# Performance work log

Measured on AMD Instinct MI355X. Metric: run time of the kernel, lower is better.

Reference implementation:

```python
import jax, jax.numpy as jnp
import numpy as np

V0, V1 = 0.1, 0.2  # SSD encode/decode variances
LEVEL_WS = [160, 80, 40, 20, 10, 5]
BOUNDS = [0, 25600, 32000, 33600, 34000, 34100, 34125]
A_TOTAL = 34125
CLS_W, LOC_W = 1.0, 2.0

def _to_cxcywh(a):
    return np.stack([(a[:, 0] + a[:, 2]) / 2.0, (a[:, 1] + a[:, 3]) / 2.0,
                     a[:, 2] - a[:, 0], a[:, 3] - a[:, 1]], 1)

def _decode(d, anc):
    xy = anc[:, :2] + d[:, :2] * V0 * anc[:, 2:]
    wh = anc[:, 2:] * np.exp(d[:, 2:] * V1)
    return np.concatenate([xy - wh / 2.0, xy + wh / 2.0], 1)

def _encode(anc, gt):
    gcx = (gt[:, 0] + gt[:, 2]) / 2.0; gcy = (gt[:, 1] + gt[:, 3]) / 2.0
    gw = gt[:, 2] - gt[:, 0]; gh = gt[:, 3] - gt[:, 1]
    return np.stack([(gcx - anc[:, 0]) / (anc[:, 2] * V0),
                     (gcy - anc[:, 1]) / (anc[:, 3] * V0),
                     np.log(np.maximum(gw, 1e-6) / anc[:, 2]) / V1,
                     np.log(np.maximum(gh, 1e-6) / anc[:, 3]) / V1], 1)

def _relabel(conf, bbox_targets, anchors):
    # Faithful mirror of the torch.no_grad() relabel loop: per-image per-level
    # decode, unique-with-counts, center-distance top-k, sigmoid-score sort,
    # scatter relabel. Data-dependent shapes, so done in numpy (no grads flow here).
    conf = np.asarray(conf); bt = np.array(bbox_targets, copy=True); anc = np.asarray(anchors)
    tanc = _to_cxcywh(anc)
    labels = bt[:, :, -1].copy()
    for b in range(conf.shape[0]):
        pos = bt[b, :, -1] == 1
        uniq = []
        for li in range(6):
            s, e = BOUNDS[li], BOUNDS[li + 1]
            m = pos[s:e]
            dec = _decode(bt[b, s:e][m][:, :4], tanc[s:e][m])
            uniq.append(np.unique(np.round(dec, 3), axis=0, return_counts=True))
        start_idx, end_idx, tmp_w = -25600, 0, 160.0
        for li, (u, c) in enumerate(uniq):
            if li > 4:
                continue
            if u.shape[0] == 0:
                continue
            max_num = int(c.max())
            start_idx += int(tmp_w ** 2); end_idx += int(tmp_w ** 2); tmp_w /= 2.0
            s, e = start_idx, end_idx
            ctr = tanc[s:e, :2]
            for ti in range(u.shape[0]):
                n_match = int(c[ti])
                if n_match == max_num:
                    continue
                gt = u[ti]
                dist = np.hypot(ctr[:, 0] - (gt[0] + gt[2]) / 2.0, ctr[:, 1] - (gt[1] + gt[3]) / 2.0)
                cand = np.argsort(dist, kind='stable')[:max_num]
                scores = 1.0 / (1.0 + np.exp(-conf[b, s + cand, 0]))
                order = np.argsort(scores, kind='stable')
                rel = cand[order[-(max_num - n_match):]] + s
                rel = rel[labels[b, rel] != 1]
                if rel.shape[0] == 0:
                    continue
                bt[b, rel, :4] = _encode(tanc[rel], np.repeat(gt[None, :], rel.shape[0], 0))
                bt[b, rel, 4] = 1.0
                labels[b, rel] = 1.0
    return labels.astype(np.float32), bt.astype(np.float32)

def _losses(conf, loc, labels, bt):
    # cls: sigmoid BCE-with-logits summed, normalized by num positives
    # loc: smooth-L1 on encoded deltas over positive anchors, same normalization
    tgt = (labels == 1).astype(conf.dtype)
    z = conf[..., 0]
    bce = jnp.maximum(z, 0) - z * tgt + jnp.log1p(jnp.exp(-jnp.abs(z)))
    num_pos = jnp.maximum(tgt.sum(), 1.0)
    cls_loss = CLS_W * bce.sum() / num_pos
    d = loc - bt[..., :4]
    sl1 = jnp.where(jnp.abs(d) < 1.0, 0.5 * d * d, jnp.abs(d) - 0.5)
    loc_loss = LOC_W * (sl1 * tgt[..., None]).sum() / num_pos
    return cls_loss, loc_loss, cls_loss + loc_loss

def setup_inputs() -> dict:
    rng = np.random.RandomState(0)
    B, NGT = 16, 8
    anchors = []
    for w in LEVEL_WS:
        stride = 640.0 / w
        t = (np.arange(w) + 0.5) * stride
        cy, cx = np.meshgrid(t, t, indexing='ij')
        cx = cx.reshape(-1); cy = cy.reshape(-1); sz = 4.0 * stride
        anchors.append(np.stack([cx - sz / 2, cy - sz / 2, cx + sz / 2, cy + sz / 2], 1))
    anchors = np.concatenate(anchors, 0).astype(np.float32)  # [34125, 4]
    tanc = _to_cxcywh(anchors)
    bt = np.zeros((B, A_TOTAL, 5), np.float32)
    bt[:, :, :4] = rng.randn(B, A_TOTAL, 4).astype(np.float32) * 0.1
    gts = np.zeros((B, NGT, 4), np.float32)
    for b in range(B):
        for g in range(NGT):
            cx, cy = rng.uniform(64, 576, 2); sz = rng.uniform(16, 256)
            gt = np.array([cx - sz / 2, cy - sz / 2, cx + sz / 2, cy + sz / 2], np.float32)
            gts[b, g] = gt
            li = int(rng.randint(0, 5))
            s, e = BOUNDS[li], BOUNDS[li + 1]
            k = int(rng.randint(2, 20))
            idx = rng.choice(e - s, size=k, replace=False) + s
            bt[b, idx, :4] = _encode(tanc[idx], np.repeat(gt[None, :], k, 0)).astype(np.float32)
            bt[b, idx, 4] = 1.0
    conf = rng.randn(B, A_TOTAL, 1).astype(np.float32)
    loc = (rng.randn(B, A_TOTAL, 4) * 0.1).astype(np.float32)
    return {"conf": jnp.asarray(conf), "loc": jnp.asarray(loc),
            "bbox_targets": jnp.asarray(bt), "anchors": jnp.asarray(anchors),
            "bbox_labels_list": jnp.asarray(gts)}

def reference(conf, loc, bbox_targets, anchors, bbox_labels_list):
    labels, bt = _relabel(conf, bbox_targets, anchors)
    return _losses(conf, loc, jnp.asarray(labels), jnp.asarray(bt))
```

## Files before the change

kernel.cpp:

```cpp
#include <hip/hip_runtime.h>
#include <cstdint>
#include <cstddef>

#define A_TOTAL 34125
#define BATCH 16
#define NBA (BATCH * A_TOTAL)
#define SBT 1024
#define PT2 25
#define NB 1024
#define CAND 768
#define NSEG (BATCH * 5)
#define CCAP 16384
#define SELGRID 160
#define SCAN_GRID 1024
#define SCAN_THR 256

__device__ __constant__ int d_bounds[7] = {0, 25600, 32000, 33600, 34000, 34100, 34125};

#define MAXU 48
#define MAXPOS 512
#define MAXC 32
#define CLAIM_NONE 0x7FFFFFFF

__global__ __launch_bounds__(SCAN_THR)
void scan_kernel(const float* __restrict__ bt,
                 const float* __restrict__ anchors,
                 const float* __restrict__ conf,
                 const float* __restrict__ loc,
                 int* __restrict__ claim,
                 uint8_t* __restrict__ posmap,
                 float* __restrict__ part,
                 int* __restrict__ ccnt,
                 int* __restrict__ done_cnt,
                 float2* __restrict__ ctr) {
    const int tid = threadIdx.x;
    const int gtid = blockIdx.x * blockDim.x + tid;
    const int gsz = gridDim.x * blockDim.x;
    if (gtid == 0) { *ccnt = 0; *done_cnt = 0; }

    int4* c4 = (int4*)claim;
    for (int i = gtid; i < NBA / 4; i += gsz)
        c4[i] = make_int4(CLAIM_NONE, CLAIM_NONE, CLAIM_NONE, CLAIM_NONE);
    for (int a = gtid; a < A_TOTAL; a += gsz) {
        const float4 ar = reinterpret_cast<const float4*>(anchors)[a];
        ctr[a] = make_float2((ar.x + ar.z) / 2.0f, (ar.y + ar.w) / 2.0f);
    }

    float bce = 0.0f, pos = 0.0f, l1 = 0.0f;

    const float4* cf4 = (const float4*)conf;
    for (int i = gtid; i < NBA / 4; i += gsz) {
        const float4 z4 = cf4[i];
        const float zz[4] = {z4.x, z4.y, z4.z, z4.w};
        #pragma unroll
        for (int c = 0; c < 4; ++c) {
            const float z = zz[c];
            bce += fmaxf(z, 0.0f) + log1pf(expf(-fabsf(z)));
        }
    }

    const float4* btv = (const float4*)bt;
    const int nchunk = NBA * 5 / 4;
    for (int f4 = gtid; f4 < nchunk; f4 += gsz) {
        const float4 v = btv[f4];
        const unsigned g0 = (unsigned)f4 * 4u;
        const unsigned m = g0 % 5u;
        if (m != 0u) {
            const unsigned c = 4u - m;
            const float val = (c == 0u) ? v.x : (c == 1u) ? v.y : (c == 2u) ? v.z : v.w;
            const unsigned i = (g0 + c) / 5u;
            const bool p = (val == 1.0f);
            posmap[i] = p ? 1 : 0;
            if (p) {
                bce -= conf[i];
                pos += 1.0f;
                const float* tp = bt + (size_t)i * 5u;
                const float4 lv4 = reinterpret_cast<const float4*>(loc)[i];
                const float dv[4] = {lv4.x - tp[0], lv4.y - tp[1],
                                     lv4.z - tp[2], lv4.w - tp[3]};
                #pragma unroll
                for (int cc = 0; cc < 4; ++cc) {
                    const float ad = fabsf(dv[cc]);
                    l1 += (ad < 1.0f) ? 0.5f * dv[cc] * dv[cc] : ad - 0.5f;
                }
            }
        }
    }

    for (int off = 32; off > 0; off >>= 1) {
        bce += __shfl_down(bce, off);
        pos += __shfl_down(pos, off);
        l1  += __shfl_down(l1, off);
    }
    __shared__ float sb[3][4];
    const int wid = tid >> 6, lane = tid & 63;
    if (lane == 0) { sb[0][wid] = bce; sb[1][wid] = pos; sb[2][wid] = l1; }
    __syncthreads();
    if (tid == 0) {
        float B = 0, P = 0, L = 0;
        #pragma unroll
        for (int w = 0; w < 4; ++w) { B += sb[0][w]; P += sb[1][w]; L += sb[2][w]; }
        part[blockIdx.x * 3 + 0] = B;
        part[blockIdx.x * 3 + 1] = P;
        part[blockIdx.x * 3 + 2] = L;
    }
}

__global__ __launch_bounds__(256)
void dedup_kernel(const float* __restrict__ bt,
                  const float* __restrict__ anchors,
                  const uint8_t* __restrict__ posmap,
                  float* __restrict__ uq,
                  int* __restrict__ uc,
                  int* __restrict__ nu_out,
                  int* __restrict__ mn_out,
                  int* __restrict__ wl,
                  int* __restrict__ wlc)
{
    const int b = blockIdx.x / 5;
    const int lv = blockIdx.x % 5;
    const int seg = blockIdx.x;
    const unsigned bA = (unsigned)b * A_TOTAL;
    const int tid = threadIdx.x;

    __shared__ int s_pos[MAXPOS];
    __shared__ float t0[MAXPOS], t1[MAXPOS], t2[MAXPOS], t3[MAXPOS];
    __shared__ int s_cnt[MAXPOS];
    __shared__ uint8_t s_rep[MAXPOS];
    __shared__ int s_ucs[MAXU];
    __shared__ int s_np, s_nu;

    if (tid == 0) { s_np = 0; s_nu = 0; }
    __syncthreads();

    {
        const unsigned gs = bA + (unsigned)d_bounds[lv];
        const unsigned ge = bA + (unsigned)d_bounds[lv + 1];
        const unsigned astart = (gs + 15u) & ~15u;
        const unsigned aend_raw = ge & ~15u;
        const unsigned hend = min(astart, ge);
        for (unsigned g = gs + tid; g < hend; g += blockDim.x)
            if (posmap[g]) {
                int p = atomicAdd(&s_np, 1);
                if (p < MAXPOS) s_pos[p] = (int)(g - bA);
            }
        if (aend_raw > astart) {
            const uint4* pm4 = (const uint4*)(posmap + astart);
            const unsigned n16 = (aend_raw - astart) >> 4;
            for (unsigned c = tid; c < n16; c += blockDim.x) {
                const uint4 v = pm4[c];
                if (v.x | v.y | v.z | v.w) {
                    const unsigned base = astart + (c << 4);
                    const unsigned wv[4] = {v.x, v.y, v.z, v.w};
                    #pragma unroll
                    for (int w = 0; w < 4; ++w) {
                        #pragma unroll
                        for (int byi = 0; byi < 4; ++byi) {
                            if ((wv[w] >> (8 * byi)) & 0xffu) {
                                int p = atomicAdd(&s_np, 1);
                                if (p < MAXPOS)
                                    s_pos[p] = (int)(base + 4u * w + byi - bA);
                            }
                        }
                    }
                }
            }
            for (unsigned g = aend_raw + tid; g < ge; g += blockDim.x)
                if (posmap[g]) {
                    int p = atomicAdd(&s_np, 1);
                    if (p < MAXPOS) s_pos[p] = (int)(g - bA);
                }
        }
    }
    __syncthreads();
    const int np_ = min(s_np, MAXPOS);

    for (int p = tid; p < np_; p += blockDim.x) {
        int a = s_pos[p];
        const float* ar = anchors + (size_t)a * 4;
        float acx = (ar[0] + ar[2]) / 2.0f;
        float acy = (ar[1] + ar[3]) / 2.0f;
        float aw = ar[2] - ar[0];
        float ah = ar[3] - ar[1];
        const float* dd = bt + ((size_t)bA + a) * 5;
        float cx = acx + (dd[0] * 0.1f) * aw;
        float cy = acy + (dd[1] * 0.1f) * ah;
        float w = aw * expf(dd[2] * 0.2f);
        float h = ah * expf(dd[3] * 0.2f);
        t0[p] = rintf((cx - w / 2.0f) * 1000.0f) / 1000.0f;
        t1[p] = rintf((cy - h / 2.0f) * 1000.0f) / 1000.0f;
        t2[p] = rintf((cx + w / 2.0f) * 1000.0f) / 1000.0f;
        t3[p] = rintf((cy + h / 2.0f) * 1000.0f) / 1000.0f;
    }
    __syncthreads();

    for (int p = tid; p < np_; p += blockDim.x) {
        const float p0 = t0[p], p1 = t1[p], p2 = t2[p], p3 = t3[p];
        int cnt = 0, firstq = np_;
        for (int q = 0; q < np_; ++q) {
            bool eq = (t0[q] == p0) && (t1[q] == p1) && (t2[q] == p2) && (t3[q] == p3);
            if (eq) { cnt++; if (q < firstq) firstq = q; }
        }
        s_cnt[p] = cnt;
        bool rep = (firstq == p);
        s_rep[p] = rep ? 1 : 0;
        if (rep) atomicAdd(&s_nu, 1);
    }
    __syncthreads();

    float* uqp = uq + (size_t)seg * MAXU * 4;
    int* ucp = uc + (size_t)seg * MAXU;
    for (int p = tid; p < np_; p += blockDim.x) {
        if (!s_rep[p]) continue;
        const float p0 = t0[p], p1 = t1[p], p2 = t2[p], p3 = t3[p];
        int rank = 0;
        for (int q = 0; q < np_; ++q) {
            if (!s_rep[q]) continue;
            float q0 = t0[q], q1 = t1[q], q2 = t2[q], q3 = t3[q];
            bool lt = (q0 < p0) || (q0 == p0 && (q1 < p1 ||
                      (q1 == p1 && (q2 < p2 || (q2 == p2 && q3 < p3)))));
            if (lt) rank++;
        }
        if (rank < MAXU) {
            uqp[rank * 4 + 0] = p0; uqp[rank * 4 + 1] = p1;
            uqp[rank * 4 + 2] = p2; uqp[rank * 4 + 3] = p3;
            ucp[rank] = s_cnt[p];
            s_ucs[rank] = s_cnt[p];
        }
    }
    __syncthreads();

    if (tid == 0) {
        const int nu = min(s_nu, MAXU);
        nu_out[seg] = nu;
        int mn = 0;
        for (int j = 0; j < nu; ++j) mn = max(mn, s_ucs[j]);
        mn_out[seg] = mn;
        int n = 0;
        for (int ti = 0; ti < nu; ++ti)
            if (s_ucs[ti] != mn) wl[seg * MAXU + n++] = seg * MAXU + ti;
        wlc[seg] = n;
    }
}

__global__ __launch_bounds__(SBT)
void select_kernel(const float* __restrict__ conf,
                   const float* __restrict__ loc,
                   const float* __restrict__ bt,
                   const float* __restrict__ anchors,
                   const float2* __restrict__ ctr,
                   const float* __restrict__ uq,
                   const int* __restrict__ uc,
                   const int* __restrict__ nu_,
                   const int* __restrict__ mn_,
                   const int* __restrict__ wl,
                   const int* __restrict__ wlc,
                   int* __restrict__ claim,
                   unsigned* __restrict__ clist,
                   int* __restrict__ ccnt,
                   int* __restrict__ done_cnt,
                   const float* __restrict__ part,
                   float* __restrict__ out) {
    const int tid = threadIdx.x;

    __shared__ int s_hist[NB];
    __shared__ unsigned long long s_cand[CAND];
    __shared__ unsigned long long s_srt[MAXC];
    __shared__ float s_sc[MAXC];
    __shared__ int s_c, s_B, s_last;

    for (int w = blockIdx.x; ; w += gridDim.x) {
        int cum = 0, ent = -1;
        for (int i = 0; i < NSEG; ++i) {
            int c = wlc[i];
            if (ent < 0 && w < cum + c) ent = wl[i * MAXU + (w - cum)];
            cum += c;
        }
        if (w >= cum) break;

        const int ti = ent % MAXU;
        const int sg = ent / MAXU;
        const int li = sg % 5;
        const int b  = sg / 5;

        int nus[5];
        #pragma unroll
        for (int l = 0; l < 5; ++l) nus[l] = nu_[b * 5 + l];

        int s = -25600;
        float tmpw = 160.0f;
        for (int l = 0; l <= li; ++l) {
            if (nus[l] != 0) { s += (int)(tmpw * tmpw); tmpw *= 0.5f; }
        }

        const int mn = mn_[sg];
        const int cnt = uc[(size_t)sg * MAXU + ti];
        const int need = mn - cnt;
        const int K = min(mn, MAXC);
        const unsigned bA = (unsigned)b * A_TOTAL;

        const float* g = uq + ((size_t)sg * MAXU + ti) * 4;
        const float gcx = (g[0] + g[2]) / 2.0f;
        const float gcy = (g[1] + g[3]) / 2.0f;

        float cxr[PT2], cyr[PT2];
        #pragma unroll
        for (int i = 0; i < PT2; ++i) {
            const float2 c = ctr[s + tid + (i << 10)];
            cxr[i] = c.x;
            cyr[i] = c.y;
        }

        s_hist[tid] = 0;
        if (tid == 0) s_c = 0;
        __syncthreads();

        #pragma unroll
        for (int i = 0; i < PT2; ++i) {
            float d = hypotf(cxr[i] - gcx, cyr[i] - gcy);
            int bin = min(NB - 1, (int)d);
            atomicAdd(&s_hist[bin], 1);
        }
        __syncthreads();

        if (tid < 64) {
            const int base = tid << 4;
            int prt[16], psum = 0;
            #pragma unroll
            for (int i = 0; i < 16; ++i) { prt[i] = s_hist[base + i]; psum += prt[i]; }
            int run = psum;
            #pragma unroll
            for (int off = 1; off < 64; off <<= 1) {
                int o = __shfl_up(run, off);
                if (tid >= off) run += o;
            }
            const int excl = run - psum;
            if (excl < K && excl + psum >= K) {
                int c = excl, bs = base + 15;
                for (int i = 0; i < 16; ++i) { c += prt[i]; if (c >= K) { bs = base + i; break; } }
                s_B = bs;
            }
        }
        __syncthreads();
        const int B = s_B;

        #pragma unroll
        for (int i = 0; i < PT2; ++i) {
            float d = hypotf(cxr[i] - gcx, cyr[i] - gcy);
            int bin = min(NB - 1, (int)d);
            if (bin <= B) {
                int p = atomicAdd(&s_c, 1);
                if (p < CAND)
                    s_cand[p] = (((unsigned long long)__float_as_uint(d)) << 32) |
                                (unsigned)(tid + (i << 10));
            }
        }
        __syncthreads();
        const int C = min(s_c, CAND);

        if (tid < C) {
            const unsigned long long mykey = s_cand[tid];
            int rank = 0;
            for (int j = 0; j < C; ++j) rank += (s_cand[j] < mykey) ? 1 : 0;
            if (rank < K) s_srt[rank] = mykey;
        }
        __syncthreads();

        if (tid < K) {
            const int o = (int)(s_srt[tid] & 0xffffffffULL);
            const float z = conf[bA + s + o];
            s_sc[tid] = 1.0f / (1.0f + expf(-z));
        }
        __syncthreads();

        if (tid < K) {
            const float my = s_sc[tid];
            int r = 0;
            for (int j = 0; j < K; ++j) {
                const float oj = s_sc[j];
                r += (oj > my || (oj == my && j > tid)) ? 1 : 0;
            }
            if (r < need) {
                const int o = (int)(s_srt[tid] & 0xffffffffULL);
                const int idx = (int)(bA + s + o);
                const int seq = li * MAXU + ti;
                atomicMin(&claim[idx], seq);
                int p = atomicAdd(ccnt, 1);
                if (p < CCAP)
                    atomicExch(&clist[p], ((unsigned)idx << 8) | (unsigned)seq);
            }
        }
        __syncthreads();
    }

    __syncthreads();
    if (tid == 0) {
        __threadfence();
        s_last = (atomicAdd(done_cnt, 1) == gridDim.x - 1) ? 1 : 0;
    }
    __syncthreads();
    if (!s_last) return;

    float bce = 0.0f, pos = 0.0f, l1 = 0.0f;
    const int cn = min(atomicAdd(ccnt, 0), CCAP);
    for (int e = tid; e < cn; e += blockDim.x) {
        const unsigned pack = atomicAdd(&clist[e], 0u);
        const int idx = (int)(pack >> 8);
        const int seq = (int)(pack & 0xffu);
        if (atomicAdd(&claim[idx], 0) != seq) continue;
        if (bt[(size_t)idx * 5 + 4] == 1.0f) continue;
        bce -= conf[idx];
        pos += 1.0f;
        const int uli = seq / MAXU;
        const int uti = seq - uli * MAXU;
        const int b = idx / A_TOTAL;
        const int a = idx - b * A_TOTAL;
        const float* g = uq + ((size_t)(b * 5 + uli) * MAXU + uti) * 4;
        const float g0 = g[0], g1 = g[1], g2 = g[2], g3 = g[3];
        const float gcx = (g0 + g2) / 2.0f, gcy = (g1 + g3) / 2.0f;
        const float gw = g2 - g0, gh = g3 - g1;
        const float* ar = anchors + (size_t)a * 4;
        const float acx = (ar[0] + ar[2]) / 2.0f;
        const float acy = (ar[1] + ar[3]) / 2.0f;
        const float aw = ar[2] - ar[0];
        const float ah = ar[3] - ar[1];
        float ep[4];
        ep[0] = (gcx - acx) / (aw * 0.1f);
        ep[1] = (gcy - acy) / (ah * 0.1f);
        ep[2] = logf(fmaxf(gw, 1e-6f) / aw) / 0.2f;
        ep[3] = logf(fmaxf(gh, 1e-6f) / ah) / 0.2f;
        const float4 lvv = reinterpret_cast<const float4*>(loc)[idx];
        const float lvf[4] = {lvv.x, lvv.y, lvv.z, lvv.w};
        #pragma unroll
        for (int c = 0; c < 4; ++c) {
            const float dd = lvf[c] - ep[c];
            const float ad = fabsf(dd);
            l1 += (ad < 1.0f) ? 0.5f * dd * dd : ad - 0.5f;
        }
    }

    if (tid < SCAN_GRID) {
        bce += part[tid * 3 + 0];
        pos += part[tid * 3 + 1];
        l1  += part[tid * 3 + 2];
    }

    for (int off = 32; off > 0; off >>= 1) {
        bce += __shfl_down(bce, off);
        pos += __shfl_down(pos, off);
        l1  += __shfl_down(l1, off);
    }
    __shared__ float sb[3][16];
    const int wid = tid >> 6, lane = tid & 63;
    if (lane == 0) { sb[0][wid] = bce; sb[1][wid] = pos; sb[2][wid] = l1; }
    __syncthreads();
    if (tid == 0) {
        float B = 0, P = 0, L = 0;
        #pragma unroll
        for (int w = 0; w < 16; ++w) { B += sb[0][w]; P += sb[1][w]; L += sb[2][w]; }
        const double a0 = (double)B;
        const double a1 = (double)P;
        const double a2 = (double)L;
        const double np_ = a1 > 1.0 ? a1 : 1.0;
        const double cls = a0 / np_;
        const double lcl = 2.0 * a2 / np_;
        out[0] = (float)cls;
        out[1] = (float)lcl;
        out[2] = (float)(cls + lcl);
    }
}

extern "C" void kernel_launch(void* const* d_in, const int* in_sizes, int n_in,
                              void* d_out, int out_size, void* d_ws, size_t ws_size,
                              hipStream_t stream) {
    const float* conf    = (const float*)d_in[0];
    const float* loc     = (const float*)d_in[1];
    const float* bt      = (const float*)d_in[2];
    const float* anchors = (const float*)d_in[3];
    float* out = (float*)d_out;

    char* ws = (char*)d_ws;
    size_t off = 0;
    int* ccnt       = (int*)(ws + off);
    int* done_cnt   = (int*)(ws + 32);     off += 64;
    float* part     = (float*)(ws + off);  off += (size_t)SCAN_GRID * 3 * sizeof(float);
    int* claim      = (int*)(ws + off);    off += (size_t)NBA * sizeof(int);
    uint8_t* posmap = (uint8_t*)(ws + off); off += ((size_t)NBA + 63) & ~63ull;
    float* uq       = (float*)(ws + off);  off += (size_t)NSEG * MAXU * 4 * sizeof(float);
    int* uc         = (int*)(ws + off);    off += (size_t)NSEG * MAXU * sizeof(int);
    int* nu_        = (int*)(ws + off);    off += (size_t)NSEG * sizeof(int);
    int* mn_        = (int*)(ws + off);    off += (size_t)NSEG * sizeof(int);
    int* wl         = (int*)(ws + off);    off += (size_t)NSEG * MAXU * sizeof(int);
    int* wlc        = (int*)(ws + off);    off += ((size_t)NSEG * sizeof(int) + 15) & ~15ull;
    unsigned* clist = (unsigned*)(ws + off); off += (size_t)CCAP * sizeof(unsigned);
    float2* ctr     = (float2*)(ws + off); off += (size_t)A_TOTAL * sizeof(float2);

    scan_kernel<<<SCAN_GRID, SCAN_THR, 0, stream>>>(bt, anchors, conf, loc, claim,
                                                    posmap, part, ccnt, done_cnt, ctr);
    dedup_kernel<<<NSEG, 256, 0, stream>>>(bt, anchors, posmap, uq, uc, nu_, mn_,
                                           wl, wlc);
    select_kernel<<<SELGRID, SBT, 0, stream>>>(conf, loc, bt, anchors, ctr, uq, uc,
                                               nu_, mn_, wl, wlc, claim, clist, ccnt,
                                               done_cnt, part, out);
}
```

Before: 57.15 us.

## Fuse scan, dedup and select kernels into one cooperative kernel with grid syncs

Merges the three separate kernel launches into a single cooperative mega-kernel of 128 blocks by 1024 threads. Grid-wide barriers replace the kernel boundaries, and the last-block done-counter finalisation becomes block 0 running after a final grid sync. This is meant to remove launch overhead and inter-kernel gaps. In exchange, the streaming scan phase now runs on fewer threads, dedup still occupies only 80 blocks, and the select phase runs on 128 blocks instead of 160.

```diff
diff --git a/kernel.cpp b/kernel.cpp
--- a/kernel.cpp
+++ b/kernel.cpp
@@ -1,19 +1,20 @@
 #include <hip/hip_runtime.h>
+#include <hip/hip_cooperative_groups.h>
 #include <cstdint>
 #include <cstddef>
+
+namespace cg = cooperative_groups;
 
 #define A_TOTAL 34125
 #define BATCH 16
 #define NBA (BATCH * A_TOTAL)
-#define SBT 1024
+#define THR 1024
+#define GRID 128
 #define PT2 25
 #define NB 1024
 #define CAND 768
 #define NSEG (BATCH * 5)
 #define CCAP 16384
-#define SELGRID 160
-#define SCAN_GRID 1024
-#define SCAN_THR 256
 
 __device__ __constant__ int d_bounds[7] = {0, 25600, 32000, 33600, 34000, 34100, 34125};
 
@@ -22,8 +23,8 @@
 #define MAXC 32
 #define CLAIM_NONE 0x7FFFFFFF
 
-__global__ __launch_bounds__(SCAN_THR)
-void scan_kernel(const float* __restrict__ bt,
+__global__ __launch_bounds__(THR)
+void mega_kernel(const float* __restrict__ bt,
                  const float* __restrict__ anchors,
                  const float* __restrict__ conf,
                  const float* __restrict__ loc,
@@ -31,97 +32,20 @@
                  uint8_t* __restrict__ posmap,
                  float* __restrict__ part,
                  int* __restrict__ ccnt,
-                 int* __restrict__ done_cnt,
-                 float2* __restrict__ ctr) {
+                 float2* __restrict__ ctr,
+                 float* __restrict__ uq,
+                 int* __restrict__ uc,
+                 int* __restrict__ nu_,
+                 int* __restrict__ mn_,
+                 int* __restrict__ wl,
+                 int* __restrict__ wlc,
+                 unsigned* __restrict__ clist,
+                 float* __restrict__ out)
+{
+    cg::grid_group grid = cg::this_grid();
     const int tid = threadIdx.x;
     const int gtid = blockIdx.x * blockDim.x + tid;
     const int gsz = gridDim.x * blockDim.x;
-    if (gtid == 0) { *ccnt = 0; *done_cnt = 0; }
-
-    int4* c4 = (int4*)claim;
-    for (int i = gtid; i < NBA / 4; i += gsz)
-        c4[i] = make_int4(CLAIM_NONE, CLAIM_NONE, CLAIM_NONE, CLAIM_NONE);
-    for (int a = gtid; a < A_TOTAL; a += gsz) {
-        const float4 ar = reinterpret_cast<const float4*>(anchors)[a];
-        ctr[a] = make_float2((ar.x + ar.z) / 2.0f, (ar.y + ar.w) / 2.0f);
-    }
-
-    float bce = 0.0f, pos = 0.0f, l1 = 0.0f;
-
-    const float4* cf4 = (const float4*)conf;
-    for (int i = gtid; i < NBA / 4; i += gsz) {
-        const float4 z4 = cf4[i];
-        const float zz[4] = {z4.x, z4.y, z4.z, z4.w};
-        #pragma unroll
-        for (int c = 0; c < 4; ++c) {
-            const float z = zz[c];
-            bce += fmaxf(z, 0.0f) + log1pf(expf(-fabsf(z)));
-        }
-    }
-
-    const float4* btv = (const float4*)bt;
-    const int nchunk = NBA * 5 / 4;
-    for (int f4 = gtid; f4 < nchunk; f4 += gsz) {
-        const float4 v = btv[f4];
-        const unsigned g0 = (unsigned)f4 * 4u;
-        const unsigned m = g0 % 5u;
-        if (m != 0u) {
-            const unsigned c = 4u - m;
-            const float val = (c == 0u) ? v.x : (c == 1u) ? v.y : (c == 2u) ? v.z : v.w;
-            const unsigned i = (g0 + c) / 5u;
-            const bool p = (val == 1.0f);
-            posmap[i] = p ? 1 : 0;
-            if (p) {
-                bce -= conf[i];
-                pos += 1.0f;
-                const float* tp = bt + (size_t)i * 5u;
-                const float4 lv4 = reinterpret_cast<const float4*>(loc)[i];
-                const float dv[4] = {lv4.x - tp[0], lv4.y - tp[1],
-                                     lv4.z - tp[2], lv4.w - tp[3]};
-                #pragma unroll
-                for (int cc = 0; cc < 4; ++cc) {
-                    const float ad = fabsf(dv[cc]);
-                    l1 += (ad < 1.0f) ? 0.5f * dv[cc] * dv[cc] : ad - 0.5f;
-                }
-            }
-        }
-    }
-
-    for (int off = 32; off > 0; off >>= 1) {
-        bce += __shfl_down(bce, off);
-        pos += __shfl_down(pos, off);
-        l1  += __shfl_down(l1, off);
-    }
-    __shared__ float sb[3][4];
-    const int wid = tid >> 6, lane = tid & 63;
-    if (lane == 0) { sb[0][wid] = bce; sb[1][wid] = pos; sb[2][wid] = l1; }
-    __syncthreads();
-    if (tid == 0) {
-        float B = 0, P = 0, L = 0;
-        #pragma unroll
-        for (int w = 0; w < 4; ++w) { B += sb[0][w]; P += sb[1][w]; L += sb[2][w]; }
-        part[blockIdx.x * 3 + 0] = B;
-        part[blockIdx.x * 3 + 1] = P;
-        part[blockIdx.x * 3 + 2] = L;
-    }
-}
-
-__global__ __launch_bounds__(256)
-void dedup_kernel(const float* __restrict__ bt,
-                  const float* __restrict__ anchors,
-                  const uint8_t* __restrict__ posmap,
-                  float* __restrict__ uq,
-                  int* __restrict__ uc,
-                  int* __restrict__ nu_out,
-                  int* __restrict__ mn_out,
-                  int* __restrict__ wl,
-                  int* __restrict__ wlc)
-{
-    const int b = blockIdx.x / 5;
-    const int lv = blockIdx.x % 5;
-    const int seg = blockIdx.x;
-    const unsigned bA = (unsigned)b * A_TOTAL;
-    const int tid = threadIdx.x;
 
     __shared__ int s_pos[MAXPOS];
     __shared__ float t0[MAXPOS], t1[MAXPOS], t2[MAXPOS], t3[MAXPOS];
@@ -129,145 +53,205 @@
     __shared__ uint8_t s_rep[MAXPOS];
     __shared__ int s_ucs[MAXU];
     __shared__ int s_np, s_nu;
-
-    if (tid == 0) { s_np = 0; s_nu = 0; }
-    __syncthreads();
+    __shared__ int s_hist[NB];
+    __shared__ unsigned long long s_cand[CAND];
+    __shared__ unsigned long long s_srt[MAXC];
+    __shared__ float s_sc[MAXC];
+    __shared__ int s_c, s_B;
+    __shared__ float sb[3][16];
+
+    if (gtid == 0) *ccnt = 0;
 
     {
-        const unsigned gs = bA + (unsigned)d_bounds[lv];
-        const unsigned ge = bA + (unsigned)d_bounds[lv + 1];
-        const unsigned astart = (gs + 15u) & ~15u;
-        const unsigned aend_raw = ge & ~15u;
-        const unsigned hend = min(astart, ge);
-        for (unsigned g = gs + tid; g < hend; g += blockDim.x)
-            if (posmap[g]) {
-                int p = atomicAdd(&s_np, 1);
-                if (p < MAXPOS) s_pos[p] = (int)(g - bA);
-            }
-        if (aend_raw > astart) {
-            const uint4* pm4 = (const uint4*)(posmap + astart);
-            const unsigned n16 = (aend_raw - astart) >> 4;
-            for (unsigned c = tid; c < n16; c += blockDim.x) {
-                const uint4 v = pm4[c];
-                if (v.x | v.y | v.z | v.w) {
-                    const unsigned base = astart + (c << 4);
-                    const unsigned wv[4] = {v.x, v.y, v.z, v.w};
+        int4* c4 = (int4*)claim;
+        for (int i = gtid; i < NBA / 4; i += gsz)
+            c4[i] = make_int4(CLAIM_NONE, CLAIM_NONE, CLAIM_NONE, CLAIM_NONE);
+        for (int a = gtid; a < A_TOTAL; a += gsz) {
+            const float4 ar = reinterpret_cast<const float4*>(anchors)[a];
+            ctr[a] = make_float2((ar.x + ar.z) / 2.0f, (ar.y + ar.w) / 2.0f);
+        }
+
+        float bce = 0.0f, pos = 0.0f, l1 = 0.0f;
+
+        const float4* cf4 = (const float4*)conf;
+        for (int i = gtid; i < NBA / 4; i += gsz) {
+            const float4 z4 = cf4[i];
+            const float zz[4] = {z4.x, z4.y, z4.z, z4.w};
+            #pragma unroll
+            for (int c = 0; c < 4; ++c) {
+                const float z = zz[c];
+                bce += fmaxf(z, 0.0f) + log1pf(expf(-fabsf(z)));
+            }
+        }
+
+        const float4* btv = (const float4*)bt;
+        const int nchunk = NBA * 5 / 4;
+        for (int f4 = gtid; f4 < nchunk; f4 += gsz) {
+            const float4 v = btv[f4];
+            const unsigned g0 = (unsigned)f4 * 4u;
+            const unsigned m = g0 % 5u;
+            if (m != 0u) {
+                const unsigned c = 4u - m;
+                const float val = (c == 0u) ? v.x : (c == 1u) ? v.y : (c == 2u) ? v.z : v.w;
+                const unsigned i = (g0 + c) / 5u;
+                const bool p = (val == 1.0f);
+                posmap[i] = p ? 1 : 0;
+                if (p) {
+                    bce -= conf[i];
+                    pos += 1.0f;
+                    const float* tp = bt + (size_t)i * 5u;
+                    const float4 lv4 = reinterpret_cast<const float4*>(loc)[i];
+                    const float dv[4] = {lv4.x - tp[0], lv4.y - tp[1],
+                                         lv4.z - tp[2], lv4.w - tp[3]};
                     #pragma unroll
-                    for (int w = 0; w < 4; ++w) {
+                    for (int cc = 0; cc < 4; ++cc) {
+                        const float ad = fabsf(dv[cc]);
+                        l1 += (ad < 1.0f) ? 0.5f * dv[cc] * dv[cc] : ad - 0.5f;
+                    }
+                }
+            }
+        }
+
+        for (int off = 32; off > 0; off >>= 1) {
+            bce += __shfl_down(bce, off);
+            pos += __shfl_down(pos, off);
+            l1  += __shfl_down(l1, off);
+        }
+        const int wid = tid >> 6, lane = tid & 63;
+        if (lane == 0) { sb[0][wid] = bce; sb[1][wid] = pos; sb[2][wid] = l1; }
+        __syncthreads();
+        if (tid == 0) {
+            float B = 0, P = 0, L = 0;
+            #pragma unroll
+            for (int w = 0; w < 16; ++w) { B += sb[0][w]; P += sb[1][w]; L += sb[2][w]; }
+            part[blockIdx.x * 3 + 0] = B;
+            part[blockIdx.x * 3 + 1] = P;
+            part[blockIdx.x * 3 + 2] = L;
+        }
+    }
+
+    grid.sync();
+
+    if (blockIdx.x < NSEG) {
+        const int b = blockIdx.x / 5;
+        const int lv = blockIdx.x % 5;
+        const int seg = blockIdx.x;
+        const unsigned bA = (unsigned)b * A_TOTAL;
+
+        if (tid == 0) { s_np = 0; s_nu = 0; }
+        __syncthreads();
+
+        {
+            const unsigned gs = bA + (unsigned)d_bounds[lv];
+            const unsigned ge = bA + (unsigned)d_bounds[lv + 1];
+            const unsigned astart = (gs + 15u) & ~15u;
+            const unsigned aend_raw = ge & ~15u;
+            const unsigned hend = min(astart, ge);
+            for (unsigned g = gs + tid; g < hend; g += blockDim.x)
+                if (posmap[g]) {
+                    int p = atomicAdd(&s_np, 1);
+                    if (p < MAXPOS) s_pos[p] = (int)(g - bA);
+                }
+            if (aend_raw > astart) {
+                const uint4* pm4 = (const uint4*)(posmap + astart);
+                const unsigned n16 = (aend_raw - astart) >> 4;
+                for (unsigned c = tid; c < n16; c += blockDim.x) {
+                    const uint4 v = pm4[c];
+                    if (v.x | v.y | v.z | v.w) {
+                        const unsigned base = astart + (c << 4);
+                        const unsigned wv[4] = {v.x, v.y, v.z, v.w};
                         #pragma unroll
-                        for (int byi = 0; byi < 4; ++byi) {
-                            if ((wv[w] >> (8 * byi)) & 0xffu) {
-                                int p = atomicAdd(&s_np, 1);
-                                if (p < MAXPOS)
-                                    s_pos[p] = (int)(base + 4u * w + byi - bA);
+                        for (int w = 0; w < 4; ++w) {
+                            #pragma unroll
+                            for (int byi = 0; byi < 4; ++byi) {
+                                if ((wv[w] >> (8 * byi)) & 0xffu) {
+                                    int p = atomicAdd(&s_np, 1);
+                                    if (p < MAXPOS)
+                                        s_pos[p] = (int)(base + 4u * w + byi - bA);
+                                }
                             }
                         }
                     }
                 }
-            }
-            for (unsigned g = aend_raw + tid; g < ge; g += blockDim.x)
-                if (posmap[g]) {
-                    int p = atomicAdd(&s_np, 1);
-                    if (p < MAXPOS) s_pos[p] = (int)(g - bA);
-                }
+                for (unsigned g = aend_raw + tid; g < ge; g += blockDim.x)
+                    if (posmap[g]) {
+                        int p = atomicAdd(&s_np, 1);
+                        if (p < MAXPOS) s_pos[p] = (int)(g - bA);
+                    }
+            }
+        }
+        __syncthreads();
+        const int np_ = min(s_np, MAXPOS);
+
+        for (int p = tid; p < np_; p += blockDim.x) {
+            int a = s_pos[p];
+            const float* ar = anchors + (size_t)a * 4;
+            float acx = (ar[0] + ar[2]) / 2.0f;
+            float acy = (ar[1] + ar[3]) / 2.0f;
+            float aw = ar[2] - ar[0];
+            float ah = ar[3] - ar[1];
+            const float* dd = bt + ((size_t)bA + a) * 5;
+            float cx = acx + (dd[0] * 0.1f) * aw;
+            float cy = acy + (dd[1] * 0.1f) * ah;
+            float w = aw * expf(dd[2] * 0.2f);
+            float h = ah * expf(dd[3] * 0.2f);
+            t0[p] = rintf((cx - w / 2.0f) * 1000.0f) / 1000.0f;
+            t1[p] = rintf((cy - h / 2.0f) * 1000.0f) / 1000.0f;
+            t2[p] = rintf((cx + w / 2.0f) * 1000.0f) / 1000.0f;
+            t3[p] = rintf((cy + h / 2.0f) * 1000.0f) / 1000.0f;
+        }
+        __syncthreads();
+
+        for (int p = tid; p < np_; p += blockDim.x) {
+            const float p0 = t0[p], p1 = t1[p], p2 = t2[p], p3 = t3[p];
+            int cnt = 0, firstq = np_;
+            for (int q = 0; q < np_; ++q) {
+                bool eq = (t0[q] == p0) && (t1[q] == p1) && (t2[q] == p2) && (t3[q] == p3);
+                if (eq) { cnt++; if (q < firstq) firstq = q; }
+            }
+            s_cnt[p] = cnt;
+            bool rep = (firstq == p);
+            s_rep[p] = rep ? 1 : 0;
+            if (rep) atomicAdd(&s_nu, 1);
+        }
+        __syncthreads();
+
+        float* uqp = uq + (size_t)seg * MAXU * 4;
+        int* ucp = uc + (size_t)seg * MAXU;
+        for (int p = tid; p < np_; p += blockDim.x) {
+            if (!s_rep[p]) continue;
+            const float p0 = t0[p], p1 = t1[p], p2 = t2[p], p3 = t3[p];
+            int rank = 0;
+            for (int q = 0; q < np_; ++q) {
+                if (!s_rep[q]) continue;
+                float q0 = t0[q], q1 = t1[q], q2 = t2[q], q3 = t3[q];
+                bool lt = (q0 < p0) || (q0 == p0 && (q1 < p1 ||
+                          (q1 == p1 && (q2 < p2 || (q2 == p2 && q3 < p3)))));
+                if (lt) rank++;
+            }
+            if (rank < MAXU) {
+                uqp[rank * 4 + 0] = p0; uqp[rank * 4 + 1] = p1;
+                uqp[rank * 4 + 2] = p2; uqp[rank * 4 + 3] = p3;
+                ucp[rank] = s_cnt[p];
+                s_ucs[rank] = s_cnt[p];
+            }
+        }
+        __syncthreads();
+
+        if (tid == 0) {
+            const int nu = min(s_nu, MAXU);
+            nu_[seg] = nu;
+            int mn = 0;
+            for (int j = 0; j < nu; ++j) mn = max(mn, s_ucs[j]);
+            mn_[seg] = mn;
+            int n = 0;
+            for (int ti = 0; ti < nu; ++ti)
+                if (s_ucs[ti] != mn) wl[seg * MAXU + n++] = seg * MAXU + ti;
+            wlc[seg] = n;
         }
     }
-    __syncthreads();
-    const int np_ = min(s_np, MAXPOS);
-
-    for (int p = tid; p < np_; p += blockDim.x) {
-        int a = s_pos[p];
-        const float* ar = anchors + (size_t)a * 4;
-        float acx = (ar[0] + ar[2]) / 2.0f;
-        float acy = (ar[1] + ar[3]) / 2.0f;
-        float aw = ar[2] - ar[0];
-        float ah = ar[3] - ar[1];
-        const float* dd = bt + ((size_t)bA + a) * 5;
-        float cx = acx + (dd[0] * 0.1f) * aw;
-        float cy = acy + (dd[1] * 0.1f) * ah;
-        float w = aw * expf(dd[2] * 0.2f);
-        float h = ah * expf(dd[3] * 0.2f);
-        t0[p] = rintf((cx - w / 2.0f) * 1000.0f) / 1000.0f;
-        t1[p] = rintf((cy - h / 2.0f) * 1000.0f) / 1000.0f;
-        t2[p] = rintf((cx + w / 2.0f) * 1000.0f) / 1000.0f;
-        t3[p] = rintf((cy + h / 2.0f) * 1000.0f) / 1000.0f;
-    }
-    __syncthreads();
-
-    for (int p = tid; p < np_; p += blockDim.x) {
-        const float p0 = t0[p], p1 = t1[p], p2 = t2[p], p3 = t3[p];
-        int cnt = 0, firstq = np_;
-        for (int q = 0; q < np_; ++q) {
-            bool eq = (t0[q] == p0) && (t1[q] == p1) && (t2[q] == p2) && (t3[q] == p3);
-            if (eq) { cnt++; if (q < firstq) firstq = q; }
-        }
-        s_cnt[p] = cnt;
-        bool rep = (firstq == p);
-        s_rep[p] = rep ? 1 : 0;
-        if (rep) atomicAdd(&s_nu, 1);
-    }
-    __syncthreads();
-
-    float* uqp = uq + (size_t)seg * MAXU * 4;
-    int* ucp = uc + (size_t)seg * MAXU;
-    for (int p = tid; p < np_; p += blockDim.x) {
-        if (!s_rep[p]) continue;
-        const float p0 = t0[p], p1 = t1[p], p2 = t2[p], p3 = t3[p];
-        int rank = 0;
-        for (int q = 0; q < np_; ++q) {
-            if (!s_rep[q]) continue;
-            float q0 = t0[q], q1 = t1[q], q2 = t2[q], q3 = t3[q];
-            bool lt = (q0 < p0) || (q0 == p0 && (q1 < p1 ||
-                      (q1 == p1 && (q2 < p2 || (q2 == p2 && q3 < p3)))));
-            if (lt) rank++;
-        }
-        if (rank < MAXU) {
-            uqp[rank * 4 + 0] = p0; uqp[rank * 4 + 1] = p1;
-            uqp[rank * 4 + 2] = p2; uqp[rank * 4 + 3] = p3;
-            ucp[rank] = s_cnt[p];
-            s_ucs[rank] = s_cnt[p];
-        }
-    }
-    __syncthreads();
-
-    if (tid == 0) {
-        const int nu = min(s_nu, MAXU);
-        nu_out[seg] = nu;
-        int mn = 0;
-        for (int j = 0; j < nu; ++j) mn = max(mn, s_ucs[j]);
-        mn_out[seg] = mn;
-        int n = 0;
-        for (int ti = 0; ti < nu; ++ti)
-            if (s_ucs[ti] != mn) wl[seg * MAXU + n++] = seg * MAXU + ti;
-        wlc[seg] = n;
-    }
-}
-
-__global__ __launch_bounds__(SBT)
-void select_kernel(const float* __restrict__ conf,
-                   const float* __restrict__ loc,
-                   const float* __restrict__ bt,
-                   const float* __restrict__ anchors,
-                   const float2* __restrict__ ctr,
-                   const float* __restrict__ uq,
-                   const int* __restrict__ uc,
-                   const int* __restrict__ nu_,
-                   const int* __restrict__ mn_,
-                   const int* __restrict__ wl,
-                   const int* __restrict__ wlc,
-                   int* __restrict__ claim,
-                   unsigned* __restrict__ clist,
-                   int* __restrict__ ccnt,
-                   int* __restrict__ done_cnt,
-                   const float* __restrict__ part,
-                   float* __restrict__ out) {
-    const int tid = threadIdx.x;
-
-    __shared__ int s_hist[NB];
-    __shared__ unsigned long long s_cand[CAND];
-    __shared__ unsigned long long s_srt[MAXC];
-    __shared__ float s_sc[MAXC];
-    __shared__ int s_c, s_B, s_last;
+
+    grid.sync();
 
     for (int w = blockIdx.x; ; w += gridDim.x) {
         int cum = 0, ent = -1;
@@ -393,80 +377,77 @@
         __syncthreads();
     }
 
-    __syncthreads();
-    if (tid == 0) {
-        __threadfence();
-        s_last = (atomicAdd(done_cnt, 1) == gridDim.x - 1) ? 1 : 0;
-    }
-    __syncthreads();
-    if (!s_last) return;
-
-    float bce = 0.0f, pos = 0.0f, l1 = 0.0f;
-    const int cn = min(atomicAdd(ccnt, 0), CCAP);
-    for (int e = tid; e < cn; e += blockDim.x) {
-        const unsigned pack = atomicAdd(&clist[e], 0u);
-        const int idx = (int)(pack >> 8);
-        const int seq = (int)(pack & 0xffu);
-        if (atomicAdd(&claim[idx], 0) != seq) continue;
-        if (bt[(size_t)idx * 5 + 4] == 1.0f) continue;
-        bce -= conf[idx];
-        pos += 1.0f;
-        const int uli = seq / MAXU;
-        const int uti = seq - uli * MAXU;
-        const int b = idx / A_TOTAL;
-        const int a = idx - b * A_TOTAL;
-        const float* g = uq + ((size_t)(b * 5 + uli) * MAXU + uti) * 4;
-        const float g0 = g[0], g1 = g[1], g2 = g[2], g3 = g[3];
-        const float gcx = (g0 + g2) / 2.0f, gcy = (g1 + g3) / 2.0f;
-        const float gw = g2 - g0, gh = g3 - g1;
-        const float* ar = anchors + (size_t)a * 4;
-        const float acx = (ar[0] + ar[2]) / 2.0f;
-        const float acy = (ar[1] + ar[3]) / 2.0f;
-        const float aw = ar[2] - ar[0];
-        const float ah = ar[3] - ar[1];
-        float ep[4];
-        ep[0] = (gcx - acx) / (aw * 0.1f);
-        ep[1] = (gcy - acy) / (ah * 0.1f);
-        ep[2] = logf(fmaxf(gw, 1e-6f) / aw) / 0.2f;
-        ep[3] = logf(fmaxf(gh, 1e-6f) / ah) / 0.2f;
-        const float4 lvv = reinterpret_cast<const float4*>(loc)[idx];
-        const float lvf[4] = {lvv.x, lvv.y, lvv.z, lvv.w};
-        #pragma unroll
-        for (int c = 0; c < 4; ++c) {
-            const float dd = lvf[c] - ep[c];
-            const float ad = fabsf(dd);
-            l1 += (ad < 1.0f) ? 0.5f * dd * dd : ad - 0.5f;
-        }
-    }
-
-    if (tid < SCAN_GRID) {
-        bce += part[tid * 3 + 0];
-        pos += part[tid * 3 + 1];
-        l1  += part[tid * 3 + 2];
-    }
-
-    for (int off = 32; off > 0; off >>= 1) {
-        bce += __shfl_down(bce, off);
-        pos += __shfl_down(pos, off);
-        l1  += __shfl_down(l1, off);
-    }
-    __shared__ float sb[3][16];
-    const int wid = tid >> 6, lane = tid & 63;
-    if (lane == 0) { sb[0][wid] = bce; sb[1][wid] = pos; sb[2][wid] = l1; }
-    __syncthreads();
-    if (tid == 0) {
-        float B = 0, P = 0, L = 0;
-        #pragma unroll
-        for (int w = 0; w < 16; ++w) { B += sb[0][w]; P += sb[1][w]; L += sb[2][w]; }
-        const double a0 = (double)B;
-        const double a1 = (double)P;
-        const double a2 = (double)L;
-        const double np_ = a1 > 1.0 ? a1 : 1.0;
-        const double cls = a0 / np_;
-        const double lcl = 2.0 * a2 / np_;
-        out[0] = (float)cls;
-        out[1] = (float)lcl;
-        out[2] = (float)(cls + lcl);
+    grid.sync();
+
+    if (blockIdx.x != 0) return;
+
+    {
+        float bce = 0.0f, pos = 0.0f, l1 = 0.0f;
+        const int cn = min(atomicAdd(ccnt, 0), CCAP);
+        for (int e = tid; e < cn; e += blockDim.x) {
+            const unsigned pack = atomicAdd(&clist[e], 0u);
+            const int idx = (int)(pack >> 8);
+            const int seq = (int)(pack & 0xffu);
+            if (atomicAdd(&claim[idx], 0) != seq) continue;
+            if (bt[(size_t)idx * 5 + 4] == 1.0f) continue;
+            bce -= conf[idx];
+            pos += 1.0f;
+            const int uli = seq / MAXU;
+            const int uti = seq - uli * MAXU;
+            const int b = idx / A_TOTAL;
+            const int a = idx - b * A_TOTAL;
+            const float* g = uq + ((size_t)(b * 5 + uli) * MAXU + uti) * 4;
+            const float g0 = g[0], g1 = g[1], g2 = g[2], g3 = g[3];
+            const float gcx = (g0 + g2) / 2.0f, gcy = (g1 + g3) / 2.0f;
+            const float gw = g2 - g0, gh = g3 - g1;
+            const float* ar = anchors + (size_t)a * 4;
+            const float acx = (ar[0] + ar[2]) / 2.0f;
+            const float acy = (ar[1] + ar[3]) / 2.0f;
+            const float aw = ar[2] - ar[0];
+            const float ah = ar[3] - ar[1];
+            float ep[4];
+            ep[0] = (gcx - acx) / (aw * 0.1f);
+            ep[1] = (gcy - acy) / (ah * 0.1f);
+            ep[2] = logf(fmaxf(gw, 1e-6f) / aw) / 0.2f;
+            ep[3] = logf(fmaxf(gh, 1e-6f) / ah) / 0.2f;
+            const float4 lvv = reinterpret_cast<const float4*>(loc)[idx];
+            const float lvf[4] = {lvv.x, lvv.y, lvv.z, lvv.w};
+            #pragma unroll
+            for (int c = 0; c < 4; ++c) {
+                const float dd = lvf[c] - ep[c];
+                const float ad = fabsf(dd);
+                l1 += (ad < 1.0f) ? 0.5f * dd * dd : ad - 0.5f;
+            }
+        }
+
+        if (tid < GRID) {
+            bce += part[tid * 3 + 0];
+            pos += part[tid * 3 + 1];
+            l1  += part[tid * 3 + 2];
+        }
+
+        for (int off = 32; off > 0; off >>= 1) {
+            bce += __shfl_down(bce, off);
+            pos += __shfl_down(pos, off);
+            l1  += __shfl_down(l1, off);
+        }
+        const int wid = tid >> 6, lane = tid & 63;
+        if (lane == 0) { sb[0][wid] = bce; sb[1][wid] = pos; sb[2][wid] = l1; }
+        __syncthreads();
+        if (tid == 0) {
+            float B = 0, P = 0, L = 0;
+            #pragma unroll
+            for (int w = 0; w < 16; ++w) { B += sb[0][w]; P += sb[1][w]; L += sb[2][w]; }
+            const double a0 = (double)B;
+            const double a1 = (double)P;
+            const double a2 = (double)L;
+            const double np_ = a1 > 1.0 ? a1 : 1.0;
+            const double cls = a0 / np_;
+            const double lcl = 2.0 * a2 / np_;
+            out[0] = (float)cls;
+            out[1] = (float)lcl;
+            out[2] = (float)(cls + lcl);
+        }
     }
 }
 
@@ -481,9 +462,8 @@
 
     char* ws = (char*)d_ws;
     size_t off = 0;
-    int* ccnt       = (int*)(ws + off);
-    int* done_cnt   = (int*)(ws + 32);     off += 64;
-    float* part     = (float*)(ws + off);  off += (size_t)SCAN_GRID * 3 * sizeof(float);
+    int* ccnt       = (int*)(ws + off);    off += 64;
+    float* part     = (float*)(ws + off);  off += (size_t)GRID * 3 * sizeof(float);
     int* claim      = (int*)(ws + off);    off += (size_t)NBA * sizeof(int);
     uint8_t* posmap = (uint8_t*)(ws + off); off += ((size_t)NBA + 63) & ~63ull;
     float* uq       = (float*)(ws + off);  off += (size_t)NSEG * MAXU * 4 * sizeof(float);
@@ -495,11 +475,12 @@
     unsigned* clist = (unsigned*)(ws + off); off += (size_t)CCAP * sizeof(unsigned);
     float2* ctr     = (float2*)(ws + off); off += (size_t)A_TOTAL * sizeof(float2);
 
-    scan_kernel<<<SCAN_GRID, SCAN_THR, 0, stream>>>(bt, anchors, conf, loc, claim,
-                                                    posmap, part, ccnt, done_cnt, ctr);
-    dedup_kernel<<<NSEG, 256, 0, stream>>>(bt, anchors, posmap, uq, uc, nu_, mn_,
-                                           wl, wlc);
-    select_kernel<<<SELGRID, SBT, 0, stream>>>(conf, loc, bt, anchors, ctr, uq, uc,
-                                               nu_, mn_, wl, wlc, claim, clist, ccnt,
-                                               done_cnt, part, out);
+    void* args[] = {
+        (void*)&bt, (void*)&anchors, (void*)&conf, (void*)&loc,
+        (void*)&claim, (void*)&posmap, (void*)&part, (void*)&ccnt, (void*)&ctr,
+        (void*)&uq, (void*)&uc, (void*)&nu_, (void*)&mn_, (void*)&wl,
+        (void*)&wlc, (void*)&clist, (void*)&out
+    };
+    hipLaunchCooperativeKernel((void*)mega_kernel, dim3(GRID), dim3(THR),
+                               args, 0, stream);
 }
```

Result: slower. 104.8 us (+83.4%).
